# Optimization experiments

Measured on AMD Instinct MI355X. Metric: run time of the kernel, lower is better.

## Reference

```python
import jax, jax.numpy as jnp
import numpy as np

N = 50000
E = 600000
IN, HID, OUT = 128, 128, 64
EPS = 1e-5

def setup_inputs() -> dict:
    key = jax.random.key(0)
    ks = jax.random.split(key, 16)
    def lin(k, i, o):
        s = 1.0 / np.sqrt(i)
        return jax.random.uniform(k, (i, o), jnp.float32, -s, s)
    inp = {
        "x": jax.random.normal(ks[0], (N, IN), jnp.float32),
        "edge_index": jax.random.randint(ks[1], (2, E), 0, N, jnp.int32),
        "edge_weight": jax.random.uniform(ks[2], (E,), jnp.float32),
        # SAGEConv params: lin_l (aggregated neighbors, with bias), lin_r (root)
        "Wl0": lin(ks[3], IN, HID), "Wr0": lin(ks[4], IN, HID), "b0": jnp.zeros((HID,), jnp.float32),
        "Wl1": lin(ks[5], HID, HID), "Wr1": lin(ks[6], HID, HID), "b1": jnp.zeros((HID,), jnp.float32),
        "Wl2": lin(ks[7], HID, OUT), "Wr2": lin(ks[8], HID, OUT), "b2": jnp.zeros((OUT,), jnp.float32),
        "gamma0": jnp.ones((HID,), jnp.float32), "beta0": jnp.zeros((HID,), jnp.float32),
        "gamma1": jnp.ones((HID,), jnp.float32), "beta1": jnp.zeros((HID,), jnp.float32),
    }
    return inp

def _sage_conv(x, src, dst, w, Wl, Wr, b):
    # weighted message m_e = w_e * x[src_e], mean-aggregated at dst
    msg = x[src] * w[:, None]                                   # [E, F]
    agg = jax.ops.segment_sum(msg, dst, num_segments=N)          # [N, F]
    cnt = jax.ops.segment_sum(jnp.ones_like(w), dst, num_segments=N)
    mean = agg / jnp.maximum(cnt, 1.0)[:, None]
    return mean @ Wl + b + x @ Wr

def _bn(x, gamma, beta):
    mu = jnp.mean(x, axis=0)
    var = jnp.var(x, axis=0)
    return (x - mu) * jax.lax.rsqrt(var + EPS) * gamma + beta

def reference(x, edge_index, edge_weight,
              Wl0, Wr0, b0, Wl1, Wr1, b1, Wl2, Wr2, b2,
              gamma0, beta0, gamma1, beta1):
    src, dst = edge_index[0], edge_index[1]
    h = _sage_conv(x, src, dst, edge_weight, Wl0, Wr0, b0)
    h = jax.nn.relu(_bn(h, gamma0, beta0))  # dropout: identity in eval
    h = _sage_conv(h, src, dst, edge_weight, Wl1, Wr1, b1)
    h = jax.nn.relu(_bn(h, gamma1, beta1))
    return _sage_conv(h, src, dst, edge_weight, Wl2, Wr2, b2)
```

## Files before the change

kernel.cpp:

```cpp
#include <hip/hip_runtime.h>
#include <hip/hip_bf16.h>

#define NN 50000
#define EE 600000
#define SREP 16
#define SLOT 64

typedef short bf16x8 __attribute__((ext_vector_type(8)));
typedef float f32x4 __attribute__((ext_vector_type(4)));

__device__ inline ushort f2bf(float x) {
  unsigned u = __float_as_uint(x);
  u = (u + 0x7fffu + ((u >> 16) & 1u)) >> 16;
  return (ushort)u;
}
__device__ inline float bflo(uint t) { return __uint_as_float(t << 16); }
__device__ inline float bfhi(uint t) { return __uint_as_float(t & 0xffff0000u); }
__device__ inline uint f22bf(float a, float b) { return ((uint)f2bf(b) << 16) | (uint)f2bf(a); }

#define FB 586
#define WB 320
#define ZN4 14560

__global__ void prep_k(const float* __restrict__ Wl0, const float* __restrict__ Wr0,
                       const float* __restrict__ Wl1, const float* __restrict__ Wr1,
                       const float* __restrict__ Wl2, const float* __restrict__ Wr2,
                       ushort* __restrict__ wbuf, int4* __restrict__ zb) {
  const int b = blockIdx.x;
  if (b < WB) {
    int idx = b * 256 + threadIdx.x;
    const float* W; int F, r, off;
    if (idx < 16384)      { W = Wl0; F = 128; r = idx;         off = 0; }
    else if (idx < 32768) { W = Wr0; F = 128; r = idx - 16384; off = 16384; }
    else if (idx < 49152) { W = Wl1; F = 128; r = idx - 32768; off = 32768; }
    else if (idx < 65536) { W = Wr1; F = 128; r = idx - 49152; off = 49152; }
    else if (idx < 73728) { W = Wl2; F = 64;  r = idx - 65536; off = 65536; }
    else                  { W = Wr2; F = 64;  r = idx - 73728; off = 73728; }
    int k = r / F, n = r % F;
    wbuf[off + n * 128 + ((((k >> 3) + n) & 15) << 3) + (k & 7)] = f2bf(W[k * F + n]);
  } else {
    int idx = (b - WB) * 256 + threadIdx.x;
    if (idx < ZN4) { int4 z = {0, 0, 0, 0}; zb[idx] = z; }
  }
}

__global__ __launch_bounds__(256) void gemm0_fill_k(
    const float* __restrict__ H, const ushort* __restrict__ Wpre,
    ushort* __restrict__ Tlb, ushort* __restrict__ Trb,
    const int* __restrict__ ei, const float* __restrict__ ew,
    int* __restrict__ cnt_d, int2* __restrict__ eL) {
  __shared__ __align__(16) ushort Wt[128 * 128];
  const int tid = threadIdx.x;
  const int b = blockIdx.x;

  if (b < FB) {
    const int base = (b * 256 + tid) * 4;
    if (base + 3 < EE) {
      int4 s4 = *(const int4*)(ei + base);
      int4 d4 = *(const int4*)(ei + EE + base);
      float4 w4 = *(const float4*)(ew + base);
      int p0 = atomicAdd(&cnt_d[d4.x], 1);
      int p1 = atomicAdd(&cnt_d[d4.y], 1);
      int p2 = atomicAdd(&cnt_d[d4.z], 1);
      int p3 = atomicAdd(&cnt_d[d4.w], 1);
      int2 r0; r0.x = s4.x; r0.y = __float_as_int(w4.x);
      int2 r1; r1.x = s4.y; r1.y = __float_as_int(w4.y);
      int2 r2; r2.x = s4.z; r2.y = __float_as_int(w4.z);
      int2 r3; r3.x = s4.w; r3.y = __float_as_int(w4.w);
      if (p0 < SLOT) eL[((size_t)d4.x << 6) + p0] = r0;
      if (p1 < SLOT) eL[((size_t)d4.y << 6) + p1] = r1;
      if (p2 < SLOT) eL[((size_t)d4.z << 6) + p2] = r2;
      if (p3 < SLOT) eL[((size_t)d4.w << 6) + p3] = r3;
    } else {
      for (int i = 0; i < 4; ++i) {
        int e = base + i;
        if (e < EE) {
          int s = ei[e], d = ei[EE + e];
          int pc = atomicAdd(&cnt_d[d], 1);
          int2 v; v.x = s; v.y = __float_as_int(ew[e]);
          if (pc < SLOT) eL[((size_t)d << 6) + pc] = v;
        }
      }
    }
    return;
  }

  const int b2 = b - FB;
  const int lane = tid & 63;
  const int w = tid >> 6;
  const int col = lane & 15;
  const int quad = lane >> 4;
  const int phase = b2 & 1;
  const int nb = (b2 >> 1) * 64;

  {
    const uint4* src = (const uint4*)(Wpre + (size_t)phase * 128 * 128);
    for (int i = tid; i < 128 * 16; i += 256) ((uint4*)Wt)[i] = src[i];
  }

  bf16x8 afrag[4];
  const int row = nb + w * 16 + col;
#pragma unroll
  for (int s = 0; s < 4; ++s) {
    const int c = s * 4 + quad;
    const int gk = c * 8;
    uint4 hv = {0, 0, 0, 0};
    float4 fa = {0.f, 0.f, 0.f, 0.f}, fb = {0.f, 0.f, 0.f, 0.f};
    if (row < NN) {
      fa = *(const float4*)(H + (size_t)row * 128 + gk);
      fb = *(const float4*)(H + (size_t)row * 128 + gk + 4);
    }
    uint* p = (uint*)&hv;
    p[0] = f22bf(fa.x, fa.y);
    p[1] = f22bf(fa.z, fa.w);
    p[2] = f22bf(fb.x, fb.y);
    p[3] = f22bf(fb.z, fb.w);
    afrag[s] = *(const bf16x8*)&hv;
  }

  __syncthreads();
  ushort* Outp = phase ? Trb : Tlb;
  const int nodeb = nb + w * 16 + quad * 4;
#pragma unroll 2
  for (int ct = 0; ct < 8; ++ct) {
    const int n = ct * 16 + col;
    f32x4 acc = {0.f, 0.f, 0.f, 0.f};
#pragma unroll
    for (int s = 0; s < 4; ++s) {
      const int c = s * 4 + quad;
      bf16x8 bfr = *(const bf16x8*)&Wt[n * 128 + (((c + n) & 15) << 3)];
      acc = __builtin_amdgcn_mfma_f32_16x16x32_bf16(afrag[s], bfr, acc, 0, 0, 0);
    }
    const int cc = ct * 16 + col;
#pragma unroll
    for (int r = 0; r < 4; ++r) {
      const int node = nodeb + r;
      if (node < NN) Outp[(size_t)node * 128 + cc] = f2bf(acc[r]);
    }
  }
}

template <int F>
__global__ __launch_bounds__(256) void gemm_mfma(
    const void* __restrict__ H, const ushort* __restrict__ Wpre,
    const float* __restrict__ statsb, const float* __restrict__ gamma,
    const float* __restrict__ beta, ushort* __restrict__ Tlb,
    ushort* __restrict__ Trb) {
  __shared__ __align__(16) ushort Wt[F * 128];
  __shared__ float ssl[256];
  const int tid = threadIdx.x;
  const int lane = tid & 63;
  const int w = tid >> 6;
  const int col = lane & 15;
  const int quad = lane >> 4;
  const int phase = blockIdx.x & 1;
  const int nb = (blockIdx.x >> 1) * 64;

  {
    float s = 0.f;
#pragma unroll 8
    for (int r = 0; r < SREP; ++r) s += statsb[r * 256 + tid];
    ssl[tid] = s;
    __syncthreads();
    if (tid < 128) {
      float mu = ssl[tid] * (1.0f / (float)NN);
      float ex2 = ssl[128 + tid] * (1.0f / (float)NN);
      float var = ex2 - mu * mu;
      float sc = gamma[tid] * rsqrtf(var + 1e-5f);
      ssl[tid] = sc;
      ssl[128 + tid] = beta[tid] - mu * sc;
    }
    __syncthreads();
  }

  {
    const uint4* src = (const uint4*)(Wpre + (size_t)phase * F * 128);
    for (int i = tid; i < F * 16; i += 256) ((uint4*)Wt)[i] = src[i];
  }

  bf16x8 afrag[4];
  const int row = nb + w * 16 + col;
#pragma unroll
  for (int s = 0; s < 4; ++s) {
    const int c = s * 4 + quad;
    const int gk = c * 8;
    uint4 hv = {0, 0, 0, 0};
    if (row < NN) hv = *(const uint4*)((const ushort*)H + (size_t)row * 128 + gk);
    uint* p = (uint*)&hv;
#pragma unroll
    for (int j = 0; j < 4; ++j) {
      float f0 = fmaxf(fmaf(bflo(p[j]), ssl[gk + 2 * j], ssl[128 + gk + 2 * j]), 0.f);
      float f1 = fmaxf(fmaf(bfhi(p[j]), ssl[gk + 2 * j + 1], ssl[128 + gk + 2 * j + 1]), 0.f);
      p[j] = f22bf(f0, f1);
    }
    afrag[s] = *(const bf16x8*)&hv;
  }

  __syncthreads();
  ushort* Outp = phase ? Trb : Tlb;
  const int nodeb = nb + w * 16 + quad * 4;
#pragma unroll 2
  for (int ct = 0; ct < F / 16; ++ct) {
    const int n = ct * 16 + col;
    f32x4 acc = {0.f, 0.f, 0.f, 0.f};
#pragma unroll
    for (int s = 0; s < 4; ++s) {
      const int c = s * 4 + quad;
      bf16x8 b = *(const bf16x8*)&Wt[n * 128 + (((c + n) & 15) << 3)];
      acc = __builtin_amdgcn_mfma_f32_16x16x32_bf16(afrag[s], b, acc, 0, 0, 0);
    }
    const int cc = ct * 16 + col;
#pragma unroll
    for (int r = 0; r < 4; ++r) {
      const int node = nodeb + r;
      if (node < NN) Outp[(size_t)node * F + cc] = f2bf(acc[r]);
    }
  }
}

template <int F, bool STATS, bool OUTF32>
__global__ __launch_bounds__(256, 8) void gather_combine(
    const ushort* __restrict__ Tlb, const int2* __restrict__ eL,
    const int* __restrict__ cnt_d, const ushort* __restrict__ Trb,
    const float* __restrict__ bias, void* __restrict__ outp,
    float* __restrict__ statsb) {
  constexpr int L = F / 2;
  constexpr int NPI = 256 / L;
  constexpr int NPB = (L == 64) ? 20 : 16;
  const int tid = threadIdx.x;
  const int cp = tid % L;
  const int c = 2 * cp;
  const int nl = tid / L;
  const int n0 = blockIdx.x * NPB;
  const float bx = bias[c], by = bias[c + 1];
  float2 S = {0.f, 0.f}, Q = {0.f, 0.f};
#pragma unroll
  for (int it = 0; it < NPB / NPI; ++it) {
    int n = n0 + it * NPI + nl;
    if constexpr (L == 64) n = __builtin_amdgcn_readfirstlane(n);
    const int deg = cnt_d[n];
    const size_t beg = (size_t)n << 6;
    float a0 = 0.f, a1 = 0.f;
    for (int base = 0; base < deg; base += L) {
      const int take = deg - base;
      int2 er = {0, 0};
      if (cp < take) er = eL[beg + base + cp];
      int m = take < L ? take : L;
      if constexpr (L == 32) m = max(m, __shfl_xor(m, 32, 64));
      int j = 0;
      for (; j + 8 <= m; j += 8) {
        int s0 = __shfl(er.x, j + 0, L);
        int s1 = __shfl(er.x, j + 1, L);
        int s2 = __shfl(er.x, j + 2, L);
        int s3 = __shfl(er.x, j + 3, L);
        int s4 = __shfl(er.x, j + 4, L);
        int s5 = __shfl(er.x, j + 5, L);
        int s6 = __shfl(er.x, j + 6, L);
        int s7 = __shfl(er.x, j + 7, L);
        float w0 = __int_as_float(__shfl(er.y, j + 0, L));
        float w1 = __int_as_float(__shfl(er.y, j + 1, L));
        float w2 = __int_as_float(__shfl(er.y, j + 2, L));
        float w3 = __int_as_float(__shfl(er.y, j + 3, L));
        float w4 = __int_as_float(__shfl(er.y, j + 4, L));
        float w5 = __int_as_float(__shfl(er.y, j + 5, L));
        float w6 = __int_as_float(__shfl(er.y, j + 6, L));
        float w7 = __int_as_float(__shfl(er.y, j + 7, L));
        uint t0 = ((const uint*)Tlb)[(size_t)s0 * L + cp];
        uint t1 = ((const uint*)Tlb)[(size_t)s1 * L + cp];
        uint t2 = ((const uint*)Tlb)[(size_t)s2 * L + cp];
        uint t3 = ((const uint*)Tlb)[(size_t)s3 * L + cp];
        uint t4 = ((const uint*)Tlb)[(size_t)s4 * L + cp];
        uint t5 = ((const uint*)Tlb)[(size_t)s5 * L + cp];
        uint t6 = ((const uint*)Tlb)[(size_t)s6 * L + cp];
        uint t7 = ((const uint*)Tlb)[(size_t)s7 * L + cp];
        a0 = fmaf(w0, bflo(t0), a0); a1 = fmaf(w0, bfhi(t0), a1);
        a0 = fmaf(w1, bflo(t1), a0); a1 = fmaf(w1, bfhi(t1), a1);
        a0 = fmaf(w2, bflo(t2), a0); a1 = fmaf(w2, bfhi(t2), a1);
        a0 = fmaf(w3, bflo(t3), a0); a1 = fmaf(w3, bfhi(t3), a1);
        a0 = fmaf(w4, bflo(t4), a0); a1 = fmaf(w4, bfhi(t4), a1);
        a0 = fmaf(w5, bflo(t5), a0); a1 = fmaf(w5, bfhi(t5), a1);
        a0 = fmaf(w6, bflo(t6), a0); a1 = fmaf(w6, bfhi(t6), a1);
        a0 = fmaf(w7, bflo(t7), a0); a1 = fmaf(w7, bfhi(t7), a1);
      }
      for (; j + 4 <= m; j += 4) {
        int s0 = __shfl(er.x, j + 0, L);
        int s1 = __shfl(er.x, j + 1, L);
        int s2 = __shfl(er.x, j + 2, L);
        int s3 = __shfl(er.x, j + 3, L);
        float w0 = __int_as_float(__shfl(er.y, j + 0, L));
        float w1 = __int_as_float(__shfl(er.y, j + 1, L));
        float w2 = __int_as_float(__shfl(er.y, j + 2, L));
        float w3 = __int_as_float(__shfl(er.y, j + 3, L));
        uint t0 = ((const uint*)Tlb)[(size_t)s0 * L + cp];
        uint t1 = ((const uint*)Tlb)[(size_t)s1 * L + cp];
        uint t2 = ((const uint*)Tlb)[(size_t)s2 * L + cp];
        uint t3 = ((const uint*)Tlb)[(size_t)s3 * L + cp];
        a0 = fmaf(w0, bflo(t0), a0); a1 = fmaf(w0, bfhi(t0), a1);
        a0 = fmaf(w1, bflo(t1), a0); a1 = fmaf(w1, bfhi(t1), a1);
        a0 = fmaf(w2, bflo(t2), a0); a1 = fmaf(w2, bfhi(t2), a1);
        a0 = fmaf(w3, bflo(t3), a0); a1 = fmaf(w3, bfhi(t3), a1);
      }
      for (; j < m; ++j) {
        int s0 = __shfl(er.x, j, L);
        float w0 = __int_as_float(__shfl(er.y, j, L));
        uint t0 = ((const uint*)Tlb)[(size_t)s0 * L + cp];
        a0 = fmaf(w0, bflo(t0), a0);
        a1 = fmaf(w0, bfhi(t0), a1);
      }
    }
    float iv = 1.0f / (float)max(deg, 1);
    uint tb = ((const uint*)Trb)[(size_t)n * L + cp];
    float2 v;
    v.x = fmaf(a0, iv, bflo(tb) + bx);
    v.y = fmaf(a1, iv, bfhi(tb) + by);
    if (OUTF32) *(float2*)((float*)outp + (size_t)n * F + c) = v;
    else ((uint*)outp)[(size_t)n * L + cp] = f22bf(v.x, v.y);
    if constexpr (STATS) {
      S.x += v.x; S.y += v.y;
      Q.x += v.x * v.x; Q.y += v.y * v.y;
    }
  }
  if constexpr (STATS) {
    __shared__ float2 sS[4][L];
    __shared__ float2 sQ[4][L];
    const int wid = tid >> 6, wl = tid & 63;
    if constexpr (L == 64) {
      sS[wid][wl] = S;
      sQ[wid][wl] = Q;
    } else {
      S.x += __shfl_xor(S.x, 32, 64); S.y += __shfl_xor(S.y, 32, 64);
      Q.x += __shfl_xor(Q.x, 32, 64); Q.y += __shfl_xor(Q.y, 32, 64);
      if (wl < 32) { sS[wid][wl] = S; sQ[wid][wl] = Q; }
    }
    __syncthreads();
    if (tid < L) {
      float2 Sa = sS[0][tid], Qa = sQ[0][tid];
#pragma unroll
      for (int w2 = 1; w2 < 4; ++w2) {
        Sa.x += sS[w2][tid].x; Sa.y += sS[w2][tid].y;
        Qa.x += sQ[w2][tid].x; Qa.y += sQ[w2][tid].y;
      }
      float* sb = statsb + (size_t)(blockIdx.x & (SREP - 1)) * 256;
      int col = 2 * tid;
      atomicAdd(&sb[col], Sa.x);
      atomicAdd(&sb[col + 1], Sa.y);
      atomicAdd(&sb[128 + col], Qa.x);
      atomicAdd(&sb[128 + col + 1], Qa.y);
    }
  }
}

extern "C" void kernel_launch(void* const* d_in, const int* in_sizes, int n_in,
                              void* d_out, int out_size, void* d_ws, size_t ws_size,
                              hipStream_t stream) {
  (void)in_sizes; (void)n_in; (void)out_size; (void)ws_size;
  const float* x   = (const float*)d_in[0];
  const int*   ei  = (const int*)d_in[1];
  const float* ew  = (const float*)d_in[2];
  const float* Wl0 = (const float*)d_in[3];
  const float* Wr0 = (const float*)d_in[4];
  const float* b0  = (const float*)d_in[5];
  const float* Wl1 = (const float*)d_in[6];
  const float* Wr1 = (const float*)d_in[7];
  const float* b1  = (const float*)d_in[8];
  const float* Wl2 = (const float*)d_in[9];
  const float* Wr2 = (const float*)d_in[10];
  const float* b2  = (const float*)d_in[11];
  const float* g0  = (const float*)d_in[12];
  const float* be0 = (const float*)d_in[13];
  const float* g1  = (const float*)d_in[14];
  const float* be1 = (const float*)d_in[15];
  float* out = (float*)d_out;

  size_t off = 0;
  auto alloc = [&](size_t b) -> void* {
    void* p = (char*)d_ws + off;
    off += (b + 255) & ~(size_t)255;
    return p;
  };
  ushort* tlb  = (ushort*)alloc((size_t)NN * 128 * 2);
  ushort* trb  = (ushort*)alloc((size_t)NN * 128 * 2);
  ushort* hpre = (ushort*)alloc((size_t)NN * 128 * 2);
  int2* eL     = (int2*)alloc((size_t)NN * SLOT * 8);
  ushort* wbuf = (ushort*)alloc(81920 * 2);
  const size_t CNT_B  = ((size_t)NN * 4 + 255) & ~(size_t)255;
  const size_t STAT_B = (size_t)SREP * 256 * 4;
  char* zb = (char*)alloc(CNT_B + 2 * STAT_B);
  int*   cnt_d   = (int*)zb;
  float* statsb0 = (float*)(zb + CNT_B);
  float* statsb1 = (float*)(zb + CNT_B + STAT_B);

  const int GEMMB = 2 * ((NN + 63) / 64);
  const int GB128 = NN / 20;
  const int GB64  = NN / 16;
  const int ZB    = (ZN4 + 255) / 256;

  prep_k<<<WB + ZB, 256, 0, stream>>>(Wl0, Wr0, Wl1, Wr1, Wl2, Wr2, wbuf, (int4*)zb);

  gemm0_fill_k<<<FB + GEMMB, 256, 0, stream>>>(x, wbuf, tlb, trb, ei, ew, cnt_d, eL);
  gather_combine<128, true, false><<<GB128, 256, 0, stream>>>(tlb, eL, cnt_d, trb, b0, hpre, statsb0);

  gemm_mfma<128><<<GEMMB, 256, 0, stream>>>(hpre, wbuf + 32768, statsb0, g0, be0, tlb, trb);
  gather_combine<128, true, false><<<GB128, 256, 0, stream>>>(tlb, eL, cnt_d, trb, b1, hpre, statsb1);

  gemm_mfma<64><<<GEMMB, 256, 0, stream>>>(hpre, wbuf + 65536, statsb1, g1, be1, tlb, trb);
  gather_combine<64, false, true><<<GB64, 256, 0, stream>>>(tlb, eL, cnt_d, trb, b2, out, nullptr);
}
```

Before: 260.0 us.

## Partition edge-list fill by destination range across block groups

The fill blocks now each scan a chunk of 8192 edges, and eight blocks share that chunk, each handling only destinations in one eighth of the node range. The intent is to keep each block's atomic counters and eL scatter writes inside a narrower address window, improving L2/MALL locality of the slot writes. The cost is that every destination index is read eight times, plus scalar source and weight loads for the matched edges.

```diff
diff --git a/kernel.cpp b/kernel.cpp
--- a/kernel.cpp
+++ b/kernel.cpp
@@ -18,7 +18,7 @@
 __device__ inline float bfhi(uint t) { return __uint_as_float(t & 0xffff0000u); }
 __device__ inline uint f22bf(float a, float b) { return ((uint)f2bf(b) << 16) | (uint)f2bf(a); }
 
-#define FB 586
+#define FB 592
 #define WB 320
 #define ZN4 14560
 
@@ -54,30 +54,32 @@
   const int b = blockIdx.x;
 
   if (b < FB) {
-    const int base = (b * 256 + tid) * 4;
-    if (base + 3 < EE) {
-      int4 s4 = *(const int4*)(ei + base);
-      int4 d4 = *(const int4*)(ei + EE + base);
-      float4 w4 = *(const float4*)(ew + base);
-      int p0 = atomicAdd(&cnt_d[d4.x], 1);
-      int p1 = atomicAdd(&cnt_d[d4.y], 1);
-      int p2 = atomicAdd(&cnt_d[d4.z], 1);
-      int p3 = atomicAdd(&cnt_d[d4.w], 1);
-      int2 r0; r0.x = s4.x; r0.y = __float_as_int(w4.x);
-      int2 r1; r1.x = s4.y; r1.y = __float_as_int(w4.y);
-      int2 r2; r2.x = s4.z; r2.y = __float_as_int(w4.z);
-      int2 r3; r3.x = s4.w; r3.y = __float_as_int(w4.w);
-      if (p0 < SLOT) eL[((size_t)d4.x << 6) + p0] = r0;
-      if (p1 < SLOT) eL[((size_t)d4.y << 6) + p1] = r1;
-      if (p2 < SLOT) eL[((size_t)d4.z << 6) + p2] = r2;
-      if (p3 < SLOT) eL[((size_t)d4.w << 6) + p3] = r3;
-    } else {
-      for (int i = 0; i < 4; ++i) {
-        int e = base + i;
-        if (e < EE) {
-          int s = ei[e], d = ei[EE + e];
-          int pc = atomicAdd(&cnt_d[d], 1);
-          int2 v; v.x = s; v.y = __float_as_int(ew[e]);
+    const int r = b & 7;
+    const int cch = b >> 3;
+    const int lo = r * (NN / 8), hi = lo + (NN / 8);
+#pragma unroll
+    for (int i = 0; i < 8; ++i) {
+      const int idx4 = cch * 2048 + i * 256 + tid;
+      const int e0 = idx4 * 4;
+      if (e0 >= EE) continue;
+      int4 d4;
+      if (e0 + 3 < EE) d4 = *(const int4*)(ei + EE + e0);
+      else {
+        d4.x = ei[EE + e0];
+        d4.y = (e0 + 1 < EE) ? ei[EE + e0 + 1] : -1;
+        d4.z = (e0 + 2 < EE) ? ei[EE + e0 + 2] : -1;
+        d4.w = (e0 + 3 < EE) ? ei[EE + e0 + 3] : -1;
+      }
+      const int dd[4] = {d4.x, d4.y, d4.z, d4.w};
+#pragma unroll
+      for (int k = 0; k < 4; ++k) {
+        const int d = dd[k];
+        if (d >= lo && d < hi) {
+          const int e = e0 + k;
+          const int pc = atomicAdd(&cnt_d[d], 1);
+          int2 v;
+          v.x = ei[e];
+          v.y = __float_as_int(ew[e]);
           if (pc < SLOT) eL[((size_t)d << 6) + pc] = v;
         }
       }
```

After: 259.6 us. About the same (-0.2%).
